# Optimization experiments

Hardware: AMD Instinct MI355X
Metric: run time of the kernel (lower is better)

The kernel has to match this reference:

```python
import jax, jax.numpy as jnp
import numpy as np

K = 3; STRIDE = 1; PAD = 1
IN_C = 256; OUT_C = 512
SPAN = K * K * IN_C        # 2304, im2col row count
M = 3                      # ALSH augmentation dims
TABLE_SIZE = 8             # hash buckets
R = 2.5                    # LSH bin width


def setup_inputs() -> dict:
    key = jax.random.key(0)
    k1, k2, k3, k4 = jax.random.split(key, 4)
    stdv = 1.0 / np.sqrt(SPAN)
    inp = jax.random.normal(k1, (16, IN_C, 56, 56), dtype=jnp.float32)
    kernels = jax.random.uniform(k2, (OUT_C, SPAN), minval=-stdv, maxval=stdv,
                                 dtype=jnp.float32)
    a_hash = jax.random.normal(k3, (SPAN + M,), dtype=jnp.float32)
    b_hash = jax.random.uniform(k4, (1,), dtype=jnp.float32) * R
    return {"input": inp, "kernels": kernels, "a_hash": a_hash,
            "b_hash": b_hash, "mode": 1}


def _P(x, m):
    # ALSH P-augmentation: append ||x||^(2^i), i=1..m, per row. x: [O, SPAN]
    n = jnp.linalg.norm(x, axis=1, keepdims=True)
    ext = jnp.concatenate([n ** (2 ** (i + 1)) for i in range(m)], axis=1)
    return jnp.concatenate([x, ext], axis=1)  # [O, SPAN+M]


def _bucket(vals, b, r, ts):
    # floor((v+b)/r) ; fmod ts ; abs  (matches torch fmod-then-abs semantics)
    idx = jnp.floor((vals + b) / r).astype(jnp.int32)
    return jnp.abs(jnp.fmod(idx, ts))


def _im2col_matr(x):
    # [N, C, H, W] -> [SPAN, N*H2*W2]
    n = x.shape[0]
    h2 = (x.shape[2] - K + 2 * PAD) // STRIDE + 1
    w2 = (x.shape[3] - K + 2 * PAD) // STRIDE + 1
    patches = jax.lax.conv_general_dilated_patches(
        x, (K, K), (STRIDE, STRIDE), [(PAD, PAD), (PAD, PAD)])  # [N, SPAN, H2, W2]
    return patches.reshape(n, SPAN, h2 * w2).transpose(1, 0, 2).reshape(SPAN, -1), h2, w2


def reference(input, kernels, a_hash, b_hash, mode):
    n = input.shape[0]
    patch_matr, h2, w2 = _im2col_matr(input)  # [SPAN, L]

    # ---- build ALSH table: bucket of each kernel row ----
    kvals = _P(kernels, M) @ a_hash           # [OUT_C]
    kbuck = _bucket(kvals, b_hash[0], R, TABLE_SIZE)

    # ---- vote: hash every unit-normalized patch column, take modal bucket ----
    unit = patch_matr / jnp.linalg.norm(patch_matr, axis=0, keepdims=True)
    q_ext = jnp.full((M, unit.shape[1]), 0.5, dtype=unit.dtype)
    votes = a_hash @ jnp.concatenate([unit, q_ext], axis=0)  # [L]
    vbuck = _bucket(votes, b_hash[0], R, TABLE_SIZE)
    counts = jnp.bincount(vbuck, length=TABLE_SIZE)
    bucket = int(jnp.argmax(counts))

    # ---- gather active kernel rows for that bucket (data-dependent) ----
    rows = np.sort(np.where(np.asarray(kbuck) == bucket)[0])
    if rows.size != 0:
        active = kernels[jnp.asarray(rows)]          # [oc, SPAN]
        out = active @ patch_matr                    # [oc, L]
        if mode:
            out = out / (float(rows.size) / OUT_C)
        oc = int(rows.size)
    else:
        out = kernels @ patch_matr
        oc = OUT_C

    out = out.reshape(oc, n, h2 * w2).transpose(1, 0, 2).reshape(n, oc, h2, w2)
    return (out, jnp.asarray(rows, dtype=jnp.int32))
```

## Files before the change

### kernel.cpp

```cpp
#include <hip/hip_runtime.h>
#include <math.h>

#define N_    16
#define C_    256
#define H_    56
#define W_    56
#define HW_   3136
#define NPIX  50176
#define OUTC  512
#define SPAN_ 2304
#define BLKPX 256
#define HBYTES 24576
#define ZOFF  (2 * HBYTES)

typedef unsigned short u16;
typedef unsigned int   u32;
typedef __attribute__((ext_vector_type(8))) short bf16x8;
typedef __attribute__((ext_vector_type(8))) unsigned short u16x8;
typedef __attribute__((ext_vector_type(4))) float f32x4;
typedef __attribute__((ext_vector_type(4))) unsigned short u16x4;

__device__ __forceinline__ u16 f2bf(float v) {
    u32 x = __float_as_uint(v);
    u32 r = (x + 0x7fffu + ((x >> 16) & 1u)) >> 16;
    return (u16)r;
}

__device__ __forceinline__ int bucketf(float v, float b) {
    int idx = (int)floorf((v + b) / 2.5f);
    int r = idx % 8;
    return r < 0 ? -r : r;
}

__global__ void kbucket_kernel(const float* __restrict__ kern,
                               const float* __restrict__ ah,
                               const float* __restrict__ bh,
                               int* __restrict__ kbuck) {
    int oc = blockIdx.x;
    const float* kr = kern + (size_t)oc * SPAN_;
    float dot = 0.f, ss = 0.f;
    for (int j = threadIdx.x; j < SPAN_; j += 64) {
        float kv = kr[j];
        dot += kv * ah[j];
        ss  += kv * kv;
    }
    for (int o = 32; o; o >>= 1) {
        dot += __shfl_down(dot, o);
        ss  += __shfl_down(ss, o);
    }
    if (threadIdx.x == 0) {
        float n2 = ss;
        float n4 = n2 * n2;
        float n8 = n4 * n4;
        float v = dot + n2 * ah[SPAN_] + n4 * ah[SPAN_ + 1] + n8 * ah[SPAN_ + 2];
        kbuck[oc] = bucketf(v, bh[0]);
    }
}

__global__ __launch_bounds__(256) void prep_fused(const float* __restrict__ x,
                                                  const float* __restrict__ ah,
                                                  u16* __restrict__ xp,
                                                  float* __restrict__ g,
                                                  float* __restrict__ s2) {
    __shared__ float aL[SPAN_];
    __shared__ u16 tl[64][68];
    __shared__ float red[4][64][10];
    int t = threadIdx.x;
    for (int j = t; j < SPAN_; j += 256) aL[j] = ah[j];

    int px0 = blockIdx.x * 64;
    int img = px0 / HW_;
    int hw0 = px0 - img * HW_;
    int px_l = t & 63;
    int cq   = t >> 6;
    float pg[9];
#pragma unroll
    for (int kk = 0; kk < 9; ++kk) pg[kk] = 0.f;
    float ps = 0.f;
    __syncthreads();

    for (int cb0 = 0; cb0 < 4; ++cb0) {
        int c0 = cb0 * 64;
#pragma unroll
        for (int rep = 0; rep < 16; ++rep) {
            int c_l = rep * 4 + cq;
            float v = x[((size_t)(img * C_ + c0 + c_l)) * HW_ + hw0 + px_l];
            tl[px_l][c_l] = f2bf(v);
            const float* ac = &aL[(c0 + c_l) * 9];
#pragma unroll
            for (int kk = 0; kk < 9; ++kk) pg[kk] += ac[kk] * v;
            ps += v * v;
        }
        __syncthreads();
        int c4  = t & 15;
        int pxs = t >> 4;
#pragma unroll
        for (int rep = 0; rep < 4; ++rep) {
            int pl = rep * 16 + pxs;
            u16x4 v4 = *(const u16x4*)(&tl[pl][c4 * 4]);
            *(u16x4*)(&xp[((size_t)(px0 + pl)) * C_ + c0 + c4 * 4]) = v4;
        }
        __syncthreads();
    }

#pragma unroll
    for (int kk = 0; kk < 9; ++kk) red[cq][px_l][kk] = pg[kk];
    red[cq][px_l][9] = ps;
    __syncthreads();
    for (int it = t; it < 640; it += 256) {
        int pl = it / 10;
        int j  = it - pl * 10;
        float s = red[0][pl][j] + red[1][pl][j] + red[2][pl][j] + red[3][pl][j];
        int q = px0 + pl;
        if (j < 9) g[(size_t)j * NPIX + q] = s;
        else       s2[q] = s;
    }
}

__global__ __launch_bounds__(256) void vote_kernel(const float* __restrict__ g,
                                                   const float* __restrict__ s2,
                                                   const float* __restrict__ ah,
                                                   const float* __restrict__ bh,
                                                   int* __restrict__ counts) {
    __shared__ int hist[8];
    if (threadIdx.x < 8) hist[threadIdx.x] = 0;
    __syncthreads();
    int q = blockIdx.x * 256 + threadIdx.x;
    int n = q / HW_;
    int p = q - n * HW_;
    int h = p / W_;
    int w = p - h * W_;
    float dot = 0.f, ss = 0.f;
#pragma unroll
    for (int kk = 0; kk < 9; ++kk) {
        int dh = kk / 3 - 1, dw = kk % 3 - 1;
        int hh = h + dh, ww = w + dw;
        if (hh >= 0 && hh < H_ && ww >= 0 && ww < W_) {
            int idx = n * HW_ + hh * W_ + ww;
            dot += g[(size_t)kk * NPIX + idx];
            ss  += s2[idx];
        }
    }
    float qext = 0.5f * (ah[SPAN_] + ah[SPAN_ + 1] + ah[SPAN_ + 2]);
    float v = dot / sqrtf(ss) + qext;
    int b = bucketf(v, bh[0]);
    atomicAdd(&hist[b], 1);
    __syncthreads();
    if (threadIdx.x < 8) atomicAdd(&counts[threadIdx.x], hist[threadIdx.x]);
}

__global__ __launch_bounds__(512) void select_kernel(const int* __restrict__ counts,
                                                     const int* __restrict__ kbuck,
                                                     int* __restrict__ rowsb,
                                                     int* __restrict__ meta,
                                                     float* __restrict__ out,
                                                     int oc_total) {
    __shared__ int sBest;
    __shared__ int sScan[512];
    int t = threadIdx.x;
    if (t == 0) {
        int best = 0, bc = counts[0];
        for (int i = 1; i < 8; ++i) {
            int c = counts[i];
            if (c > bc) { bc = c; best = i; }
        }
        sBest = best;
    }
    __syncthreads();
    int best = sBest;
    int flag = (kbuck[t] == best) ? 1 : 0;
    sScan[t] = flag;
    __syncthreads();
    for (int off = 1; off < 512; off <<= 1) {
        int add = (t >= off) ? sScan[t - off] : 0;
        __syncthreads();
        sScan[t] += add;
        __syncthreads();
    }
    int cnt = sScan[511];
    int pos = sScan[t] - flag;
    if (flag) rowsb[pos] = t;
    if (cnt == 0) rowsb[t] = t;
    else if (t >= cnt) rowsb[t] = 0;
    if (t == 0) {
        meta[0] = cnt;
        meta[1] = (cnt == 0) ? OUTC : cnt;
    }
    float* rout = out + (size_t)N_ * oc_total * HW_;
    int eff = (cnt == 0) ? OUTC : cnt;
    int nw = eff < oc_total ? eff : oc_total;
    if (cnt == 0) {
        if (t < nw) rout[t] = (float)t;
    } else if (flag && pos < nw) {
        rout[pos] = (float)t;
    }
}

__global__ __launch_bounds__(256) void prep_w(const float* __restrict__ kern,
                                              const int* __restrict__ rowsb,
                                              const int* __restrict__ meta,
                                              const int* __restrict__ mode,
                                              u16* __restrict__ wfrag, int nf4) {
    int e = blockIdx.x * 256 + threadIdx.x;
    int lane = e & 63;
    int t2 = e >> 6;
    int g = t2 % nf4;
    int s = t2 / nf4;
    int kk = s >> 3;
    int cb = s & 7;
    int q = lane >> 4;
    int mcol = lane & 15;
    int ocEff = meta[1];
    int cnt = meta[0];
    float scale = (mode[0] && cnt > 0) ? 512.0f / (float)cnt : 1.0f;
    int oc_i = g * 16 + mcol;
    bool valid = oc_i < ocEff;
    int row = valid ? rowsb[oc_i] : 0;
    const float* kr = kern + (size_t)row * SPAN_;
    u16 w8[8];
#pragma unroll
    for (int j = 0; j < 8; ++j) {
        int c = cb * 32 + q * 8 + j;
        float v = valid ? kr[c * 9 + kk] * scale : 0.f;
        w8[j] = f2bf(v);
    }
    u16* dst = wfrag + ((size_t)((s * nf4 + g) * 64 + lane)) * 8;
#pragma unroll
    for (int j = 0; j < 8; ++j) dst[j] = w8[j];
}

__global__ __launch_bounds__(256, 3) void conv_mfma(const u16* __restrict__ xp,
                                                    const u16* __restrict__ wfrag,
                                                    float* __restrict__ out,
                                                    int nf4, int oc_total, int nby) {
    __shared__ char halo[2 * HBYTES + 64];

    int flat = blockIdx.x;
    int bx, by;
    int full = 192 * nby;
    if (flat < full) {
        int gsz = 8 * nby;
        int gi = flat / gsz;
        int tr = flat - gi * gsz;
        by = tr >> 3;
        bx = gi * 8 + (tr & 7);
    } else {
        int tr = flat - full;
        by = tr >> 2;
        bx = 192 + (tr & 3);
    }

    const int t = threadIdx.x;
    const int lane = t & 63;
    const int wv = t >> 6;
    const int pb = bx * BLKPX;
    const int fb = by * 4;
    const int lane15 = lane & 15;
    const int laneq  = lane >> 4;

    if (t < 4) *(u16x8*)&halo[ZOFF + t * 16] = (u16x8){0,0,0,0,0,0,0,0};

    u32 valMask[4];
    int aB[4][3];
#pragma unroll
    for (int f = 0; f < 4; ++f) {
        int p = pb + wv * 64 + f * 16 + lane15;
        int img = p / HW_;
        int rp = p - img * HW_;
        int h = rp / W_;
        int w = rp - h * W_;
        u32 m = 0;
#pragma unroll
        for (int kk = 0; kk < 9; ++kk) {
            int dh = kk / 3 - 1, dw = kk % 3 - 1;
            int hh = h + dh, ww = w + dw;
            if (hh >= 0 && hh < H_ && ww >= 0 && ww < W_) m |= (1u << kk);
        }
        valMask[f] = m;
#pragma unroll
        for (int j = 0; j < 3; ++j) {
            int sn = 57 + wv * 64 + f * 16 + lane15 + (j - 1);
            aB[f][j] = sn * 64 + ((laneq ^ ((sn >> 1) & 3)) << 4);
        }
    }

    f32x4 acc[4][4];
#pragma unroll
    for (int f = 0; f < 4; ++f)
#pragma unroll
        for (int gg = 0; gg < 4; ++gg) acc[f][gg] = (f32x4){0.f, 0.f, 0.f, 0.f};

    const char* xpb = (const char*)xp;
    const int q4 = (((t & 3) ^ ((t >> 3) & 3)) << 4);
    int gpx[6];
#pragma unroll
    for (int r = 0; r < 6; ++r) {
        int p = pb - 57 + r * 64 + (t >> 2);
        gpx[r] = p < 0 ? 0 : (p >= NPIX ? NPIX - 1 : p);
    }

#pragma unroll
    for (int r = 0; r < 6; ++r)
        __builtin_amdgcn_global_load_lds(
            (const __attribute__((address_space(1))) unsigned int*)
                (xpb + (size_t)gpx[r] * 512 + q4),
            (__attribute__((address_space(3))) unsigned int*)&halo[r * 4096 + t * 16],
            16, 0, 0);

    const size_t cbStride = (size_t)nf4 * 512;
    const size_t kkStride = cbStride * 8;
    const u16* wl = wfrag + (size_t)fb * 512 + (size_t)lane * 8;
    bf16x8 bB[3][4];
#define LOADB(slot, cb_, kk_) do {                                              \
    const u16* _wp = wl + (size_t)(kk_) * kkStride + (size_t)(cb_) * cbStride;  \
    _Pragma("unroll")                                                           \
    for (int _g = 0; _g < 4; ++_g)                                              \
        bB[slot][_g] = *(const bf16x8*)(_wp + (size_t)_g * 512);                \
} while (0)

    LOADB(0, 0, 0);
    LOADB(1, 0, 1);

    for (int cb = 0; cb < 8; ++cb) {
        __syncthreads();
        const int hoff = (cb & 1) * HBYTES;

        if (cb < 7) {
            const int nb = ((cb + 1) & 1) * HBYTES;
#pragma unroll
            for (int r = 0; r < 6; ++r)
                __builtin_amdgcn_global_load_lds(
                    (const __attribute__((address_space(1))) unsigned int*)
                        (xpb + (size_t)gpx[r] * 512 + (cb + 1) * 64 + q4),
                    (__attribute__((address_space(3))) unsigned int*)
                        &halo[nb + r * 4096 + t * 16],
                    16, 0, 0);
        }

#pragma unroll
        for (int kk = 0; kk < 9; ++kk) {
            if (kk < 7)            LOADB((kk + 2) % 3, cb, kk + 2);
            else if (cb < 7)       LOADB((kk + 2) % 3, cb + 1, kk - 7);

            const int dh = kk / 3 - 1;
            const int j  = kk % 3;
            const int toffH = hoff + dh * 3584;
            bf16x8 aX[4];
#pragma unroll
            for (int f = 0; f < 4; ++f) {
                int addr = ((valMask[f] >> kk) & 1) ? (aB[f][j] + toffH) : ZOFF;
                aX[f] = *(const bf16x8*)&halo[addr];
            }
#pragma unroll
            for (int gg = 0; gg < 4; ++gg)
#pragma unroll
                for (int f = 0; f < 4; ++f)
                    acc[f][gg] = __builtin_amdgcn_mfma_f32_16x16x32_bf16(
                        aX[f], bB[kk % 3][gg], acc[f][gg], 0, 0, 0);
        }
    }
#undef LOADB

#pragma unroll
    for (int f = 0; f < 4; ++f) {
        int p0 = pb + wv * 64 + f * 16 + laneq * 4;
        int img0 = p0 / HW_;
        int hw0 = p0 - img0 * HW_;
#pragma unroll
        for (int gg = 0; gg < 4; ++gg) {
            int oc = (fb + gg) * 16 + lane15;
            if (oc < oc_total) {
                float* op = out + ((size_t)img0 * oc_total + oc) * HW_ + hw0;
                *(f32x4*)op = acc[f][gg];
            }
        }
    }
}

extern "C" void kernel_launch(void* const* d_in, const int* in_sizes, int n_in,
                              void* d_out, int out_size, void* d_ws, size_t ws_size,
                              hipStream_t stream) {
    const float* x    = (const float*)d_in[0];
    const float* kern = (const float*)d_in[1];
    const float* ah   = (const float*)d_in[2];
    const float* bh   = (const float*)d_in[3];
    const int*   mode = (const int*)d_in[4];
    float* out = (float*)d_out;

    int oc_total = (out_size % (N_ * HW_ + 1) == 0) ? out_size / (N_ * HW_ + 1)
                                                    : OUTC;
    int nfTot = (oc_total + 15) / 16;
    int nf4   = ((nfTot + 3) / 4) * 4;
    int nby   = nf4 / 4;

    u16*   xp     = (u16*)d_ws;
    u16*   wfrag  = xp + (size_t)NPIX * C_;
    float* g      = (float*)(wfrag + (size_t)72 * 32 * 64 * 8);
    float* s2     = g + (size_t)9 * NPIX;
    int*   counts = (int*)(s2 + NPIX);
    int*   kbuck  = counts + 8;
    int*   rowsb  = kbuck + OUTC;
    int*   meta   = rowsb + OUTC;

    hipMemsetAsync(counts, 0, 8 * sizeof(int), stream);

    prep_fused<<<NPIX / 64, 256, 0, stream>>>(x, ah, xp, g, s2);

    kbucket_kernel<<<OUTC, 64, 0, stream>>>(kern, ah, bh, kbuck);
    vote_kernel<<<NPIX / 256, 256, 0, stream>>>(g, s2, ah, bh, counts);
    select_kernel<<<1, 512, 0, stream>>>(counts, kbuck, rowsb, meta, out, oc_total);

    prep_w<<<18 * nf4, 256, 0, stream>>>(kern, rowsb, meta, mode, wfrag, nf4);

    conv_mfma<<<(NPIX / BLKPX) * nby, 256, 0, stream>>>(xp, wfrag, out, nf4,
                                                        oc_total, nby);
}
```

Baseline: 113.5 us.

## Fuse kbucket into prep and select into prep_w; retile conv to 3 output fragments

Folds the kernel-row hashing into extra blocks of prep_fused and moves the bucket argmax/scan into every prep_w block, which removes two launches and the rowsb/meta round trip through global memory. In conv_mfma each block now covers 3 output-channel fragments instead of 4. The B operand moves from a 3-slot ring to a single next-slot prefetch, and padding zeros come from a register select instead of a zero LDS slot. Launch bounds drop to 2 blocks per CU. The smaller tile raises weight and halo reloads per useful MFMA and changes the grid shape. Recomputing the scan in every prep_w block adds redundant work.

```diff
diff --git a/kernel.cpp b/kernel.cpp
--- a/kernel.cpp
+++ b/kernel.cpp
@@ -11,7 +11,6 @@
 #define SPAN_ 2304
 #define BLKPX 256
 #define HBYTES 24576
-#define ZOFF  (2 * HBYTES)
 
 typedef unsigned short u16;
 typedef unsigned int   u32;
@@ -32,40 +31,44 @@
     return r < 0 ? -r : r;
 }
 
-__global__ void kbucket_kernel(const float* __restrict__ kern,
-                               const float* __restrict__ ah,
-                               const float* __restrict__ bh,
-                               int* __restrict__ kbuck) {
-    int oc = blockIdx.x;
-    const float* kr = kern + (size_t)oc * SPAN_;
-    float dot = 0.f, ss = 0.f;
-    for (int j = threadIdx.x; j < SPAN_; j += 64) {
-        float kv = kr[j];
-        dot += kv * ah[j];
-        ss  += kv * kv;
-    }
-    for (int o = 32; o; o >>= 1) {
-        dot += __shfl_down(dot, o);
-        ss  += __shfl_down(ss, o);
-    }
-    if (threadIdx.x == 0) {
-        float n2 = ss;
-        float n4 = n2 * n2;
-        float n8 = n4 * n4;
-        float v = dot + n2 * ah[SPAN_] + n4 * ah[SPAN_ + 1] + n8 * ah[SPAN_ + 2];
-        kbuck[oc] = bucketf(v, bh[0]);
-    }
-}
-
 __global__ __launch_bounds__(256) void prep_fused(const float* __restrict__ x,
                                                   const float* __restrict__ ah,
+                                                  const float* __restrict__ bh,
+                                                  const float* __restrict__ kern,
                                                   u16* __restrict__ xp,
                                                   float* __restrict__ g,
-                                                  float* __restrict__ s2) {
+                                                  float* __restrict__ s2,
+                                                  int* __restrict__ kbuck) {
+    int kb = blockIdx.x - (NPIX / 64);
+    int t = threadIdx.x;
+    if (kb >= 0) {
+        int oc_l = t >> 2, part = t & 3;
+        int oc = kb * 64 + oc_l;
+        const float* kr = kern + (size_t)oc * SPAN_ + part * 576;
+        const float* ap = ah + part * 576;
+        float dot = 0.f, ss = 0.f;
+        for (int i = 0; i < 144; ++i) {
+            float4 kv = *(const float4*)(kr + i * 4);
+            float4 av = *(const float4*)(ap + i * 4);
+            dot += kv.x * av.x + kv.y * av.y + kv.z * av.z + kv.w * av.w;
+            ss  += kv.x * kv.x + kv.y * kv.y + kv.z * kv.z + kv.w * kv.w;
+        }
+        dot += __shfl_xor(dot, 1); dot += __shfl_xor(dot, 2);
+        ss  += __shfl_xor(ss, 1);  ss  += __shfl_xor(ss, 2);
+        if (part == 0) {
+            float n2 = ss;
+            float n4 = n2 * n2;
+            float n8 = n4 * n4;
+            float v = dot + n2 * ah[SPAN_] + n4 * ah[SPAN_ + 1] +
+                      n8 * ah[SPAN_ + 2];
+            kbuck[oc] = bucketf(v, bh[0]);
+        }
+        return;
+    }
+
     __shared__ float aL[SPAN_];
     __shared__ u16 tl[64][68];
     __shared__ float red[4][64][10];
-    int t = threadIdx.x;
     for (int j = t; j < SPAN_; j += 256) aL[j] = ah[j];
 
     int px0 = blockIdx.x * 64;
@@ -149,73 +152,72 @@
     if (threadIdx.x < 8) atomicAdd(&counts[threadIdx.x], hist[threadIdx.x]);
 }
 
-__global__ __launch_bounds__(512) void select_kernel(const int* __restrict__ counts,
-                                                     const int* __restrict__ kbuck,
-                                                     int* __restrict__ rowsb,
-                                                     int* __restrict__ meta,
-                                                     float* __restrict__ out,
-                                                     int oc_total) {
-    __shared__ int sBest;
-    __shared__ int sScan[512];
+__global__ __launch_bounds__(256) void prep_w(const float* __restrict__ kern,
+                                              const int* __restrict__ kbuck,
+                                              const int* __restrict__ counts,
+                                              const int* __restrict__ mode,
+                                              float* __restrict__ out,
+                                              u16* __restrict__ wfrag,
+                                              int nfB, int oc_total) {
+    __shared__ int sc[256];
+    __shared__ int rowsL[512];
     int t = threadIdx.x;
-    if (t == 0) {
-        int best = 0, bc = counts[0];
-        for (int i = 1; i < 8; ++i) {
-            int c = counts[i];
-            if (c > bc) { bc = c; best = i; }
-        }
-        sBest = best;
-    }
-    __syncthreads();
-    int best = sBest;
-    int flag = (kbuck[t] == best) ? 1 : 0;
-    sScan[t] = flag;
-    __syncthreads();
-    for (int off = 1; off < 512; off <<= 1) {
-        int add = (t >= off) ? sScan[t - off] : 0;
+    int best = 0, bc = counts[0];
+#pragma unroll
+    for (int i = 1; i < 8; ++i) {
+        int c = counts[i];
+        if (c > bc) { bc = c; best = i; }
+    }
+    int f0 = (kbuck[t] == best) ? 1 : 0;
+    int f1 = (kbuck[t + 256] == best) ? 1 : 0;
+    sc[t] = f0 | (f1 << 16);
+    __syncthreads();
+    for (int off = 1; off < 256; off <<= 1) {
+        int add = (t >= off) ? sc[t - off] : 0;
         __syncthreads();
-        sScan[t] += add;
+        sc[t] += add;
         __syncthreads();
     }
-    int cnt = sScan[511];
-    int pos = sScan[t] - flag;
-    if (flag) rowsb[pos] = t;
-    if (cnt == 0) rowsb[t] = t;
-    else if (t >= cnt) rowsb[t] = 0;
-    if (t == 0) {
-        meta[0] = cnt;
-        meta[1] = (cnt == 0) ? OUTC : cnt;
-    }
-    float* rout = out + (size_t)N_ * oc_total * HW_;
-    int eff = (cnt == 0) ? OUTC : cnt;
-    int nw = eff < oc_total ? eff : oc_total;
-    if (cnt == 0) {
-        if (t < nw) rout[t] = (float)t;
-    } else if (flag && pos < nw) {
-        rout[pos] = (float)t;
-    }
-}
-
-__global__ __launch_bounds__(256) void prep_w(const float* __restrict__ kern,
-                                              const int* __restrict__ rowsb,
-                                              const int* __restrict__ meta,
-                                              const int* __restrict__ mode,
-                                              u16* __restrict__ wfrag, int nf4) {
-    int e = blockIdx.x * 256 + threadIdx.x;
+    int tot = sc[255];
+    int t0  = tot & 0xffff;
+    int cnt = t0 + (tot >> 16);
+    int pos0 = (sc[t] & 0xffff) - f0;
+    int pos1 = t0 + (sc[t] >> 16) - f1;
+    rowsL[t] = 0; rowsL[t + 256] = 0;
+    __syncthreads();
+    if (cnt == 0) { rowsL[t] = t; rowsL[t + 256] = t + 256; }
+    else {
+        if (f0) rowsL[pos0] = t;
+        if (f1) rowsL[pos1] = t + 256;
+    }
+    __syncthreads();
+    int ocEff = (cnt == 0) ? OUTC : cnt;
+    float scale = (mode[0] && cnt > 0) ? 512.0f / (float)cnt : 1.0f;
+
+    if (blockIdx.x == 0) {
+        float* rout = out + (size_t)N_ * oc_total * HW_;
+        int nw = ocEff < oc_total ? ocEff : oc_total;
+        if (cnt == 0) {
+            if (t < nw) rout[t] = (float)t;
+            if (t + 256 < nw) rout[t + 256] = (float)(t + 256);
+        } else {
+            if (f0 && pos0 < nw) rout[pos0] = (float)t;
+            if (f1 && pos1 < nw) rout[pos1] = (float)(t + 256);
+        }
+    }
+
+    int e = blockIdx.x * 256 + t;
     int lane = e & 63;
     int t2 = e >> 6;
-    int g = t2 % nf4;
-    int s = t2 / nf4;
+    int g = t2 % nfB;
+    int s = t2 / nfB;
     int kk = s >> 3;
     int cb = s & 7;
     int q = lane >> 4;
     int mcol = lane & 15;
-    int ocEff = meta[1];
-    int cnt = meta[0];
-    float scale = (mode[0] && cnt > 0) ? 512.0f / (float)cnt : 1.0f;
     int oc_i = g * 16 + mcol;
     bool valid = oc_i < ocEff;
-    int row = valid ? rowsb[oc_i] : 0;
+    int row = valid ? rowsL[oc_i] : 0;
     const float* kr = kern + (size_t)row * SPAN_;
     u16 w8[8];
 #pragma unroll
@@ -224,16 +226,16 @@
         float v = valid ? kr[c * 9 + kk] * scale : 0.f;
         w8[j] = f2bf(v);
     }
-    u16* dst = wfrag + ((size_t)((s * nf4 + g) * 64 + lane)) * 8;
+    u16* dst = wfrag + ((size_t)((s * nfB + g) * 64 + lane)) * 8;
 #pragma unroll
     for (int j = 0; j < 8; ++j) dst[j] = w8[j];
 }
 
-__global__ __launch_bounds__(256, 3) void conv_mfma(const u16* __restrict__ xp,
+__global__ __launch_bounds__(256, 2) void conv_mfma(const u16* __restrict__ xp,
                                                     const u16* __restrict__ wfrag,
                                                     float* __restrict__ out,
-                                                    int nf4, int oc_total, int nby) {
-    __shared__ char halo[2 * HBYTES + 64];
+                                                    int nfB, int oc_total, int nby) {
+    __shared__ char halo[2 * HBYTES];
 
     int flat = blockIdx.x;
     int bx, by;
@@ -254,11 +256,9 @@
     const int lane = t & 63;
     const int wv = t >> 6;
     const int pb = bx * BLKPX;
-    const int fb = by * 4;
+    const int fb = by * 3;
     const int lane15 = lane & 15;
     const int laneq  = lane >> 4;
-
-    if (t < 4) *(u16x8*)&halo[ZOFF + t * 16] = (u16x8){0,0,0,0,0,0,0,0};
 
     u32 valMask[4];
     int aB[4][3];
@@ -280,15 +280,16 @@
 #pragma unroll
         for (int j = 0; j < 3; ++j) {
             int sn = 57 + wv * 64 + f * 16 + lane15 + (j - 1);
-            aB[f][j] = sn * 64 + ((laneq ^ ((sn >> 1) & 3)) << 4);
-        }
-    }
-
-    f32x4 acc[4][4];
+            aB[f][j] = sn * 64 + ((laneq ^ ((sn >> 1) & 3)) << 4) - 3584;
+        }
+    }
+
+    f32x4 acc[4][3];
 #pragma unroll
     for (int f = 0; f < 4; ++f)
 #pragma unroll
-        for (int gg = 0; gg < 4; ++gg) acc[f][gg] = (f32x4){0.f, 0.f, 0.f, 0.f};
+        for (int gg = 0; gg < 3; ++gg) acc[f][gg] = (f32x4){0.f, 0.f, 0.f, 0.f};
+    const bf16x8 zf = {0, 0, 0, 0, 0, 0, 0, 0};
 
     const char* xpb = (const char*)xp;
     const int q4 = (((t & 3) ^ ((t >> 3) & 3)) << 4);
@@ -307,23 +308,22 @@
             (__attribute__((address_space(3))) unsigned int*)&halo[r * 4096 + t * 16],
             16, 0, 0);
 
-    const size_t cbStride = (size_t)nf4 * 512;
+    const size_t cbStride = (size_t)nfB * 512;
     const size_t kkStride = cbStride * 8;
     const u16* wl = wfrag + (size_t)fb * 512 + (size_t)lane * 8;
-    bf16x8 bB[3][4];
-#define LOADB(slot, cb_, kk_) do {                                              \
+    bf16x8 bW[3], bWn[3];
+#define LOADB(dst, cb_, kk_) do {                                               \
     const u16* _wp = wl + (size_t)(kk_) * kkStride + (size_t)(cb_) * cbStride;  \
     _Pragma("unroll")                                                           \
-    for (int _g = 0; _g < 4; ++_g)                                              \
-        bB[slot][_g] = *(const bf16x8*)(_wp + (size_t)_g * 512);                \
+    for (int _g = 0; _g < 3; ++_g)                                              \
+        dst[_g] = *(const bf16x8*)(_wp + (size_t)_g * 512);                     \
 } while (0)
 
-    LOADB(0, 0, 0);
-    LOADB(1, 0, 1);
-
+    LOADB(bW, 0, 0);
+
+#pragma unroll
     for (int cb = 0; cb < 8; ++cb) {
         __syncthreads();
-        const int hoff = (cb & 1) * HBYTES;
 
         if (cb < 7) {
             const int nb = ((cb + 1) & 1) * HBYTES;
@@ -339,24 +339,28 @@
 
 #pragma unroll
         for (int kk = 0; kk < 9; ++kk) {
-            if (kk < 7)            LOADB((kk + 2) % 3, cb, kk + 2);
-            else if (cb < 7)       LOADB((kk + 2) % 3, cb + 1, kk - 7);
+            if (kk < 8)       LOADB(bWn, cb, kk + 1);
+            else if (cb < 7)  LOADB(bWn, cb + 1, 0);
 
             const int dh = kk / 3 - 1;
             const int j  = kk % 3;
-            const int toffH = hoff + dh * 3584;
+            const int IMM = (cb & 1) * HBYTES + (dh + 1) * 3584;
             bf16x8 aX[4];
 #pragma unroll
             for (int f = 0; f < 4; ++f) {
-                int addr = ((valMask[f] >> kk) & 1) ? (aB[f][j] + toffH) : ZOFF;
-                aX[f] = *(const bf16x8*)&halo[addr];
+                bf16x8 a = *(const bf16x8*)&halo[aB[f][j] + IMM];
+                aX[f] = ((valMask[f] >> kk) & 1) ? a : zf;
             }
 #pragma unroll
-            for (int gg = 0; gg < 4; ++gg)
+            for (int gg = 0; gg < 3; ++gg)
 #pragma unroll
                 for (int f = 0; f < 4; ++f)
                     acc[f][gg] = __builtin_amdgcn_mfma_f32_16x16x32_bf16(
-                        aX[f], bB[kk % 3][gg], acc[f][gg], 0, 0, 0);
+                        aX[f], bW[gg], acc[f][gg], 0, 0, 0);
+            if (kk < 8 || cb < 7) {
+#pragma unroll
+                for (int gg = 0; gg < 3; ++gg) bW[gg] = bWn[gg];
+            }
         }
     }
 #undef LOADB
@@ -367,7 +371,7 @@
         int img0 = p0 / HW_;
         int hw0 = p0 - img0 * HW_;
 #pragma unroll
-        for (int gg = 0; gg < 4; ++gg) {
+        for (int gg = 0; gg < 3; ++gg) {
             int oc = (fb + gg) * 16 + lane15;
             if (oc < oc_total) {
                 float* op = out + ((size_t)img0 * oc_total + oc) * HW_ + hw0;
@@ -390,28 +394,23 @@
     int oc_total = (out_size % (N_ * HW_ + 1) == 0) ? out_size / (N_ * HW_ + 1)
                                                     : OUTC;
     int nfTot = (oc_total + 15) / 16;
-    int nf4   = ((nfTot + 3) / 4) * 4;
-    int nby   = nf4 / 4;
+    int nby   = (nfTot + 2) / 3;
+    int nfB   = nby * 3;
 
     u16*   xp     = (u16*)d_ws;
     u16*   wfrag  = xp + (size_t)NPIX * C_;
-    float* g      = (float*)(wfrag + (size_t)72 * 32 * 64 * 8);
+    float* g      = (float*)(wfrag + (size_t)72 * 36 * 64 * 8);
     float* s2     = g + (size_t)9 * NPIX;
     int*   counts = (int*)(s2 + NPIX);
     int*   kbuck  = counts + 8;
-    int*   rowsb  = kbuck + OUTC;
-    int*   meta   = rowsb + OUTC;
 
     hipMemsetAsync(counts, 0, 8 * sizeof(int), stream);
 
-    prep_fused<<<NPIX / 64, 256, 0, stream>>>(x, ah, xp, g, s2);
-
-    kbucket_kernel<<<OUTC, 64, 0, stream>>>(kern, ah, bh, kbuck);
+    prep_fused<<<NPIX / 64 + 8, 256, 0, stream>>>(x, ah, bh, kern, xp, g, s2,
+                                                  kbuck);
     vote_kernel<<<NPIX / 256, 256, 0, stream>>>(g, s2, ah, bh, counts);
-    select_kernel<<<1, 512, 0, stream>>>(counts, kbuck, rowsb, meta, out, oc_total);
-
-    prep_w<<<18 * nf4, 256, 0, stream>>>(kern, rowsb, meta, mode, wfrag, nf4);
-
-    conv_mfma<<<(NPIX / BLKPX) * nby, 256, 0, stream>>>(xp, wfrag, out, nf4,
+    prep_w<<<18 * nfB, 256, 0, stream>>>(kern, kbuck, counts, mode, out, wfrag,
+                                         nfB, oc_total);
+    conv_mfma<<<(NPIX / BLKPX) * nby, 256, 0, stream>>>(xp, wfrag, out, nfB,
                                                         oc_total, nby);
 }
```

Result: faster. 106.6 us (-6.0%).
